# Performance work log

Hardware: AMD Instinct MI355X
Metric: run time of the kernel (lower is better)

Reference implementation:

```python
import jax, jax.numpy as jnp
import numpy as np

N = 100000
E = 3200000
IN_F = 256
OUT_F = 128
ALPHA = 0.2  # LeakyReLU negative slope


def setup_inputs() -> dict:
    key = jax.random.key(0)
    k1, k2, k3, k4, k5 = jax.random.split(key, 5)
    x = jax.random.normal(k1, (N, IN_F), dtype=jnp.float32)
    edge_row = jax.random.randint(k2, (E,), 0, N, dtype=jnp.int32)
    edge_col = jax.random.randint(k3, (E,), 0, N, dtype=jnp.int32)
    # xavier-uniform style scaling (gain 1.414)
    lim_W = 1.414 * np.sqrt(6.0 / (IN_F + OUT_F))
    W = jax.random.uniform(k4, (IN_F, OUT_F), minval=-lim_W, maxval=lim_W, dtype=jnp.float32)
    lim_a = 1.414 * np.sqrt(6.0 / (1 + 2 * OUT_F))
    a = jax.random.uniform(k5, (2 * OUT_F,), minval=-lim_a, maxval=lim_a, dtype=jnp.float32)
    return {"x": x, "edge_row": edge_row, "edge_col": edge_col, "W": W, "a": a}


def reference(x, edge_row, edge_col, W, a):
    # h = x @ W : [N, OUT_F]
    h = x @ W
    # edge score: leakyrelu([h_src || h_dst] . a) computed as two node-level dots
    a_src, a_dst = a[:OUT_F], a[OUT_F:]
    s_src = h @ a_src  # [N]
    s_dst = h @ a_dst  # [N]
    e = s_src[edge_row] + s_dst[edge_col]  # [E]
    e = jnp.where(e > 0, e, ALPHA * e)     # LeakyReLU
    # sparse softmax along dim=1 (over columns within each row -> segment by row)
    row_max = jax.ops.segment_max(e, edge_row, num_segments=N)  # [N]
    e_exp = jnp.exp(e - row_max[edge_row])
    row_sum = jax.ops.segment_sum(e_exp, edge_row, num_segments=N)  # [N]
    att = e_exp / row_sum[edge_row]  # [E]
    # sparse-dense matmul: h_prime[i] = sum_j att_ij * h[j]
    h_prime = jax.ops.segment_sum(att[:, None] * h[edge_col], edge_row, num_segments=N)
    # concat=True -> ELU
    return jax.nn.elu(h_prime)
```

## Files before the change

kernel.cpp:

```cpp
#include <hip/hip_runtime.h>
#include <hip/hip_bf16.h>
#include <math.h>

#define N_NODES 100000
#define N_EDGES 3200000
#define IN_FEAT 256
#define OUT_FEAT 128
#define ALPHA 0.2f
#define NB 782
#define NBLK 200
#define CHUNK 16000

#define SCAN_N (NB * NBLK)
#define SCAN_ELEMS 2048
#define SCAN_BLOCKS ((SCAN_N + SCAN_ELEMS - 1) / SCAN_ELEMS)
#define SCAT_IT 10

typedef __attribute__((ext_vector_type(8))) short short8;
typedef __attribute__((ext_vector_type(4))) float f32x4;

__device__ __forceinline__ ushort f2bf(float f) {
  __hip_bfloat16 h = __float2bfloat16(f);
  return __builtin_bit_cast(ushort, h);
}
__device__ __forceinline__ float bflo(uint u) { return __uint_as_float(u << 16); }
__device__ __forceinline__ float bfhi(uint u) { return __uint_as_float(u & 0xFFFF0000u); }

__global__ __launch_bounds__(256) void wt_kernel(const float* __restrict__ W,
                                                 ushort* __restrict__ Wt) {
  int id = blockIdx.x * 256 + threadIdx.x;
  int c = id >> 8;
  int k = id & 255;
  Wt[id] = f2bf(W[k * OUT_FEAT + c]);
}

#define GBM 128
#define GBK 32
#define A_LD 40
#define C_LD 136
#define HIST_BLKS NBLK

__global__ __launch_bounds__(256) void gemm_hist_kernel(const float* __restrict__ x,
                                                        const ushort* __restrict__ Wt,
                                                        const float* __restrict__ a,
                                                        const int* __restrict__ erow,
                                                        ushort* __restrict__ h16,
                                                        float* __restrict__ s_src,
                                                        float* __restrict__ s_dst,
                                                        int* __restrict__ G) {
  __shared__ union {
    struct { ushort A[GBM * A_LD]; ushort B[OUT_FEAT * A_LD]; } s;
    ushort C[GBM * C_LD];
    int hist[NB];
  } sm;
  __shared__ float sa[2 * OUT_FEAT];
  const int tid = threadIdx.x;

  if (blockIdx.x < HIST_BLKS) {
    const int b = blockIdx.x;
    for (int k = tid; k < NB; k += 256) sm.hist[k] = 0;
    __syncthreads();
    const int base = b * CHUNK;
    for (int i = base + tid; i < base + CHUNK; i += 256) atomicAdd(&sm.hist[erow[i] >> 7], 1);
    __syncthreads();
    for (int k = tid; k < NB; k += 256) G[k * NBLK + b] = sm.hist[k];
    return;
  }

  const int row0 = (blockIdx.x - HIST_BLKS) * GBM;
  const int lane = tid & 63;
  const int wave = tid >> 6;
  const int lr = lane & 15;
  const int lg = lane >> 4;

  sa[tid] = a[tid];

  f32x4 acc[2][8];
#pragma unroll
  for (int m = 0; m < 2; ++m)
#pragma unroll
    for (int n = 0; n < 8; ++n) acc[m][n] = (f32x4)(0.f);

  const int sr = tid >> 1;
  const int sh = tid & 1;
  const bool arow_ok = (row0 + sr) < N_NODES;
  const float* xg = x + (size_t)(row0 + sr) * IN_FEAT + sh * 16;
  const ushort* wg = Wt + sr * IN_FEAT + sh * 16;

  for (int ks = 0; ks < IN_FEAT / GBK; ++ks) {
    float4 f[4];
    if (arow_ok) {
#pragma unroll
      for (int i = 0; i < 4; ++i) f[i] = *(const float4*)(xg + ks * GBK + i * 4);
    } else {
#pragma unroll
      for (int i = 0; i < 4; ++i) f[i] = make_float4(0.f, 0.f, 0.f, 0.f);
    }
#pragma unroll
    for (int i = 0; i < 4; ++i) {
      uint2 p;
      p.x = (uint)f2bf(f[i].x) | ((uint)f2bf(f[i].y) << 16);
      p.y = (uint)f2bf(f[i].z) | ((uint)f2bf(f[i].w) << 16);
      *(uint2*)&sm.s.A[sr * A_LD + sh * 16 + i * 4] = p;
    }
    {
      short8 b0 = *(const short8*)(wg + ks * GBK);
      short8 b1 = *(const short8*)(wg + ks * GBK + 8);
      *(short8*)&sm.s.B[sr * A_LD + sh * 16] = b0;
      *(short8*)&sm.s.B[sr * A_LD + sh * 16 + 8] = b1;
    }
    __syncthreads();
    short8 af[2], bf[8];
#pragma unroll
    for (int m = 0; m < 2; ++m)
      af[m] = *(const short8*)&sm.s.A[(wave * 32 + m * 16 + lr) * A_LD + lg * 8];
#pragma unroll
    for (int n = 0; n < 8; ++n)
      bf[n] = *(const short8*)&sm.s.B[(n * 16 + lr) * A_LD + lg * 8];
#pragma unroll
    for (int m = 0; m < 2; ++m)
#pragma unroll
      for (int n = 0; n < 8; ++n)
        acc[m][n] = __builtin_amdgcn_mfma_f32_16x16x32_bf16(af[m], bf[n], acc[m][n], 0, 0, 0);
    __syncthreads();
  }

#pragma unroll
  for (int m = 0; m < 2; ++m)
#pragma unroll
    for (int n = 0; n < 8; ++n)
#pragma unroll
      for (int i = 0; i < 4; ++i)
        sm.C[(wave * 32 + m * 16 + lg * 4 + i) * C_LD + n * 16 + lr] = f2bf(acc[m][n][i]);
  __syncthreads();
  {
    const int row = sr;
    const bool ok = (row0 + row) < N_NODES;
    const ushort* src = &sm.C[row * C_LD + sh * 64];
    if (ok) {
      ushort* dst = h16 + (size_t)(row0 + row) * OUT_FEAT + sh * 64;
#pragma unroll
      for (int i = 0; i < 8; ++i) *(short8*)(dst + i * 8) = *(const short8*)(src + i * 8);
    }
    float ds = 0.f, dd = 0.f;
    const float* as = &sa[sh * 64];
    const float* ad = &sa[OUT_FEAT + sh * 64];
#pragma unroll
    for (int i = 0; i < 64; ++i) {
      float hv = __uint_as_float((uint)src[i] << 16);
      ds = fmaf(hv, as[i], ds);
      dd = fmaf(hv, ad[i], dd);
    }
    ds += __shfl_xor(ds, 1, 64);
    dd += __shfl_xor(dd, 1, 64);
    if (sh == 0 && ok) {
      s_src[row0 + row] = ds;
      s_dst[row0 + row] = dd;
    }
  }
}

__global__ __launch_bounds__(256) void scan1_kernel(const int* __restrict__ src,
                                                    int* __restrict__ dst,
                                                    int* __restrict__ bsum) {
  __shared__ int tsum[256];
  const int b = blockIdx.x;
  const int t = threadIdx.x;
  const int base = b * SCAN_ELEMS + t * 8;
  int v[8];
  int s = 0;
#pragma unroll
  for (int i = 0; i < 8; ++i) {
    int idx = base + i;
    v[i] = (idx < SCAN_N) ? src[idx] : 0;
    s += v[i];
  }
  tsum[t] = s;
  __syncthreads();
  for (int d = 1; d < 256; d <<= 1) {
    int u = (t >= d) ? tsum[t - d] : 0;
    __syncthreads();
    tsum[t] += u;
    __syncthreads();
  }
  int run = (t == 0) ? 0 : tsum[t - 1];
#pragma unroll
  for (int i = 0; i < 8; ++i) {
    int idx = base + i;
    if (idx < SCAN_N) dst[idx] = run;
    run += v[i];
  }
  if (t == 255) bsum[b] = tsum[255];
}

__global__ __launch_bounds__(256) void scan3_kernel(int* __restrict__ dst,
                                                    const int* __restrict__ bsum) {
  __shared__ int s[128];
  const int b = blockIdx.x;
  const int t = threadIdx.x;
  if (t < 128) s[t] = (t < SCAN_BLOCKS) ? bsum[t] : 0;
  __syncthreads();
  for (int d = 1; d < 128; d <<= 1) {
    int u = 0;
    if (t >= d && t < 128) u = s[t - d];
    __syncthreads();
    if (t < 128) s[t] += u;
    __syncthreads();
  }
  const int add = (b == 0) ? 0 : s[b - 1];
  const int base = b * SCAN_ELEMS + t * 8;
#pragma unroll
  for (int i = 0; i < 8; ++i) {
    int idx = base + i;
    if (idx < SCAN_N) dst[idx] += add;
  }
  if (b == 0 && t == 0) dst[SCAN_N] = s[SCAN_BLOCKS - 1];
}

__global__ __launch_bounds__(1024) void partition_kernel(const int* __restrict__ erow,
                                                         const int* __restrict__ ecol,
                                                         const int* __restrict__ scanG,
                                                         uint* __restrict__ packed) {
  __shared__ int cur[NB];
  const int b = blockIdx.x;
  const int t = threadIdx.x;
  for (int k = t; k < NB; k += 1024) cur[k] = scanG[k * NBLK + b];
  __syncthreads();
  const int base = b * CHUNK;
  for (int i = base + t; i < base + CHUNK; i += 1024) {
    int r = erow[i];
    int c = ecol[i];
    int pos = atomicAdd(&cur[r >> 7], 1);
    packed[pos] = ((uint)(r & 127) << 17) | (uint)c;
  }
}

__global__ __launch_bounds__(512) void bucket_scatter_kernel(const uint* __restrict__ packed,
                                                             const int* __restrict__ scanG,
                                                             int* __restrict__ offs,
                                                             int* __restrict__ scol) {
  __shared__ int cnt[128];
  __shared__ int sc[128];
  const int b = blockIdx.x;
  const int t = threadIdx.x;
  const int beg = scanG[b * NBLK];
  const int end = scanG[(b + 1) * NBLK];
  if (t < 128) cnt[t] = 0;
  __syncthreads();
  uint it[SCAT_IT];
  int nit = 0;
#pragma unroll
  for (int k = 0; k < SCAT_IT; ++k) {
    int i = beg + t + k * 512;
    if (i < end) {
      uint p = packed[i];
      it[k] = p;
      nit = k + 1;
      atomicAdd(&cnt[p >> 17], 1);
    }
  }
  __syncthreads();
  if (t < 128) sc[t] = cnt[t];
  __syncthreads();
  for (int d = 1; d < 128; d <<= 1) {
    int v = 0;
    if (t >= d && t < 128) v = sc[t - d];
    __syncthreads();
    if (t < 128) sc[t] += v;
    __syncthreads();
  }
  const int row0 = b << 7;
  if (t < 128) {
    int rstart = beg + sc[t] - cnt[t];
    if (row0 + t < N_NODES) offs[row0 + t] = rstart;
    sc[t] = rstart;
    cnt[t] = 0;
  }
  if (b == NB - 1 && t == 0) offs[N_NODES] = end;
  __syncthreads();
#pragma unroll
  for (int k = 0; k < SCAT_IT; ++k) {
    if (k < nit) {
      uint p = it[k];
      int rl = p >> 17;
      int pos = sc[rl] + atomicAdd(&cnt[rl], 1);
      scol[pos] = (int)(p & 0x1FFFFu);
    }
  }
}

__global__ __launch_bounds__(256) void attn_kernel(const ushort* __restrict__ h16,
                                                   const float* __restrict__ s_src,
                                                   const float* __restrict__ s_dst,
                                                   const int* __restrict__ offs,
                                                   const int* __restrict__ scol,
                                                   float* __restrict__ out) {
  __shared__ uint2 apair[4][128];
  const int lane = threadIdx.x & 63;
  const int w = threadIdx.x >> 6;
  const int r = blockIdx.x * 4 + w;
  const int o0 = offs[r];
  const int deg = offs[r + 1] - o0;
  const int g = lane >> 4;
  const int fo = (lane & 15) * 8;
  float* orow = out + (size_t)r * OUT_FEAT + fo;

  if (deg == 0) {
    if (g == 0) {
      *(float4*)orow = make_float4(0.f, 0.f, 0.f, 0.f);
      *(float4*)(orow + 4) = make_float4(0.f, 0.f, 0.f, 0.f);
    }
    return;
  }

  const float ssrc = s_src[r];
  const ushort* hb = h16 + fo;
  float acc[8] = {0.f, 0.f, 0.f, 0.f, 0.f, 0.f, 0.f, 0.f};

  if (deg <= 128) {
    int c0 = 0, c1 = 0;
    float p0 = -INFINITY, p1 = -INFINITY;
    if (lane < deg) {
      c0 = scol[o0 + lane];
      float e = ssrc + s_dst[c0];
      p0 = e > 0.f ? e : ALPHA * e;
    }
    if (lane + 64 < deg) {
      c1 = scol[o0 + 64 + lane];
      float e = ssrc + s_dst[c1];
      p1 = e > 0.f ? e : ALPHA * e;
    }
    float m = fmaxf(p0, p1);
#pragma unroll
    for (int off = 32; off >= 1; off >>= 1) m = fmaxf(m, __shfl_xor(m, off, 64));
    p0 = __expf(p0 - m);
    p1 = __expf(p1 - m);
    float ssum = p0 + p1;
#pragma unroll
    for (int off = 32; off >= 1; off >>= 1) ssum += __shfl_xor(ssum, off, 64);
    const float inv = 1.f / ssum;
    p0 *= inv;
    p1 *= inv;

    apair[w][lane] = make_uint2(__float_as_uint(p0), (uint)c0);
    apair[w][64 + lane] = make_uint2(__float_as_uint(p1), (uint)c1);

    const int degR = (deg + 3) & ~3;
#pragma unroll 4
    for (int j = 0; j < degR; j += 4) {
      uint2 pr = apair[w][j + g];
      float att = __uint_as_float(pr.x);
      uint4 v = *(const uint4*)(hb + (size_t)pr.y * OUT_FEAT);
      acc[0] = fmaf(att, bflo(v.x), acc[0]);
      acc[1] = fmaf(att, bfhi(v.x), acc[1]);
      acc[2] = fmaf(att, bflo(v.y), acc[2]);
      acc[3] = fmaf(att, bfhi(v.y), acc[3]);
      acc[4] = fmaf(att, bflo(v.z), acc[4]);
      acc[5] = fmaf(att, bfhi(v.z), acc[5]);
      acc[6] = fmaf(att, bflo(v.w), acc[6]);
      acc[7] = fmaf(att, bfhi(v.w), acc[7]);
    }
  } else {
    float m = -INFINITY;
    for (int j = lane; j < deg; j += 64) {
      int c = scol[o0 + j];
      float e = ssrc + s_dst[c];
      e = e > 0.f ? e : ALPHA * e;
      m = fmaxf(m, e);
    }
#pragma unroll
    for (int off = 32; off >= 1; off >>= 1) m = fmaxf(m, __shfl_xor(m, off, 64));
    float ssum = 0.f;
    for (int j = lane; j < deg; j += 64) {
      int c = scol[o0 + j];
      float e = ssrc + s_dst[c];
      e = e > 0.f ? e : ALPHA * e;
      ssum += __expf(e - m);
    }
#pragma unroll
    for (int off = 32; off >= 1; off >>= 1) ssum += __shfl_xor(ssum, off, 64);
    const float inv = 1.f / ssum;
    for (int j = 0; j < deg; j += 4) {
      int jj = j + g;
      float att = 0.f;
      int c = 0;
      if (jj < deg) {
        c = scol[o0 + jj];
        float e = ssrc + s_dst[c];
        e = e > 0.f ? e : ALPHA * e;
        att = __expf(e - m) * inv;
      }
      uint4 v = *(const uint4*)(hb + (size_t)c * OUT_FEAT);
      acc[0] = fmaf(att, bflo(v.x), acc[0]);
      acc[1] = fmaf(att, bfhi(v.x), acc[1]);
      acc[2] = fmaf(att, bflo(v.y), acc[2]);
      acc[3] = fmaf(att, bfhi(v.y), acc[3]);
      acc[4] = fmaf(att, bflo(v.z), acc[4]);
      acc[5] = fmaf(att, bfhi(v.z), acc[5]);
      acc[6] = fmaf(att, bflo(v.w), acc[6]);
      acc[7] = fmaf(att, bfhi(v.w), acc[7]);
    }
  }

#pragma unroll
  for (int k = 0; k < 8; ++k) {
    acc[k] += __shfl_xor(acc[k], 16, 64);
    acc[k] += __shfl_xor(acc[k], 32, 64);
  }
  if (g == 0) {
#pragma unroll
    for (int k = 0; k < 8; ++k) acc[k] = acc[k] > 0.f ? acc[k] : expm1f(acc[k]);
    *(float4*)orow = make_float4(acc[0], acc[1], acc[2], acc[3]);
    *(float4*)(orow + 4) = make_float4(acc[4], acc[5], acc[6], acc[7]);
  }
}

extern "C" void kernel_launch(void* const* d_in, const int* in_sizes, int n_in,
                              void* d_out, int out_size, void* d_ws, size_t ws_size,
                              hipStream_t stream) {
  const float* x = (const float*)d_in[0];
  const int* erow = (const int*)d_in[1];
  const int* ecol = (const int*)d_in[2];
  const float* W = (const float*)d_in[3];
  const float* a = (const float*)d_in[4];
  float* out = (float*)d_out;

  char* ws = (char*)d_ws;
  size_t off = 0;
  auto alloc = [&](size_t bytes) {
    void* p = ws + off;
    off = (off + bytes + 255) & ~(size_t)255;
    return p;
  };
  const int M_PAD = 782 * GBM;
  ushort* h16 = (ushort*)alloc((size_t)M_PAD * OUT_FEAT * sizeof(ushort));
  ushort* Wt = (ushort*)alloc((size_t)IN_FEAT * OUT_FEAT * sizeof(ushort));
  float* s_src = (float*)alloc((size_t)N_NODES * sizeof(float));
  float* s_dst = (float*)alloc((size_t)N_NODES * sizeof(float));
  int* offs = (int*)alloc((size_t)(N_NODES + 1) * sizeof(int));
  int* G = (int*)alloc((size_t)SCAN_N * sizeof(int));
  int* scanG = (int*)alloc((size_t)(SCAN_N + 1) * sizeof(int));
  int* bsum = (int*)alloc((size_t)SCAN_BLOCKS * sizeof(int));
  uint* packed = (uint*)alloc((size_t)N_EDGES * sizeof(uint));
  int* scol = (int*)alloc((size_t)N_EDGES * sizeof(int));

  wt_kernel<<<(IN_FEAT * OUT_FEAT) / 256, 256, 0, stream>>>(W, Wt);
  gemm_hist_kernel<<<HIST_BLKS + 782, 256, 0, stream>>>(x, Wt, a, erow, h16, s_src, s_dst, G);
  scan1_kernel<<<SCAN_BLOCKS, 256, 0, stream>>>(G, scanG, bsum);
  scan3_kernel<<<SCAN_BLOCKS, 256, 0, stream>>>(scanG, bsum);
  partition_kernel<<<NBLK, 1024, 0, stream>>>(erow, ecol, scanG, packed);
  bucket_scatter_kernel<<<NB, 512, 0, stream>>>(packed, scanG, offs, scol);
  attn_kernel<<<N_NODES / 4, 256, 0, stream>>>(h16, s_src, s_dst, offs, scol, out);
}
```

Measured before the change: 214.4 us.

## Keep full W tile in LDS, load x fragments directly to registers

Result: slower. 274.8 us (+28.2%).

```diff
diff --git a/kernel.cpp b/kernel.cpp
--- a/kernel.cpp
+++ b/kernel.cpp
@@ -26,6 +26,15 @@
 __device__ __forceinline__ float bflo(uint u) { return __uint_as_float(u << 16); }
 __device__ __forceinline__ float bfhi(uint u) { return __uint_as_float(u & 0xFFFF0000u); }
 
+__device__ __forceinline__ short8 pack_bf8(float4 a, float4 b) {
+  union { short8 s; uint u[4]; } r;
+  r.u[0] = (uint)f2bf(a.x) | ((uint)f2bf(a.y) << 16);
+  r.u[1] = (uint)f2bf(a.z) | ((uint)f2bf(a.w) << 16);
+  r.u[2] = (uint)f2bf(b.x) | ((uint)f2bf(b.y) << 16);
+  r.u[3] = (uint)f2bf(b.z) | ((uint)f2bf(b.w) << 16);
+  return r.s;
+}
+
 __global__ __launch_bounds__(256) void wt_kernel(const float* __restrict__ W,
                                                  ushort* __restrict__ Wt) {
   int id = blockIdx.x * 256 + threadIdx.x;
@@ -36,7 +45,7 @@
 
 #define GBM 128
 #define GBK 32
-#define A_LD 40
+#define B_LD 264
 #define C_LD 136
 #define HIST_BLKS NBLK
 
@@ -49,7 +58,7 @@
                                                         float* __restrict__ s_dst,
                                                         int* __restrict__ G) {
   __shared__ union {
-    struct { ushort A[GBM * A_LD]; ushort B[OUT_FEAT * A_LD]; } s;
+    ushort B[OUT_FEAT * B_LD];
     ushort C[GBM * C_LD];
     int hist[NB];
   } sm;
@@ -75,56 +84,47 @@
 
   sa[tid] = a[tid];
 
+  for (int i = tid; i < (OUT_FEAT * IN_FEAT) / 8; i += 256) {
+    int col = i >> 5;
+    int kc = (i & 31) << 3;
+    *(short8*)&sm.B[col * B_LD + kc] = *(const short8*)(Wt + col * IN_FEAT + kc);
+  }
+  __syncthreads();
+
   f32x4 acc[2][8];
 #pragma unroll
   for (int m = 0; m < 2; ++m)
 #pragma unroll
     for (int n = 0; n < 8; ++n) acc[m][n] = (f32x4)(0.f);
 
-  const int sr = tid >> 1;
-  const int sh = tid & 1;
-  const bool arow_ok = (row0 + sr) < N_NODES;
-  const float* xg = x + (size_t)(row0 + sr) * IN_FEAT + sh * 16;
-  const ushort* wg = Wt + sr * IN_FEAT + sh * 16;
-
+  const int arow0 = row0 + wave * 32 + lr;
+  const int arow1 = arow0 + 16;
+  const float* xg0 = x + (size_t)arow0 * IN_FEAT + lg * 8;
+  const float* xg1 = x + (size_t)arow1 * IN_FEAT + lg * 8;
+  const bool ok0 = arow0 < N_NODES;
+  const bool ok1 = arow1 < N_NODES;
+  const float4 z4 = make_float4(0.f, 0.f, 0.f, 0.f);
+
+#pragma unroll
   for (int ks = 0; ks < IN_FEAT / GBK; ++ks) {
-    float4 f[4];
-    if (arow_ok) {
-#pragma unroll
-      for (int i = 0; i < 4; ++i) f[i] = *(const float4*)(xg + ks * GBK + i * 4);
-    } else {
-#pragma unroll
-      for (int i = 0; i < 4; ++i) f[i] = make_float4(0.f, 0.f, 0.f, 0.f);
-    }
-#pragma unroll
-    for (int i = 0; i < 4; ++i) {
-      uint2 p;
-      p.x = (uint)f2bf(f[i].x) | ((uint)f2bf(f[i].y) << 16);
-      p.y = (uint)f2bf(f[i].z) | ((uint)f2bf(f[i].w) << 16);
-      *(uint2*)&sm.s.A[sr * A_LD + sh * 16 + i * 4] = p;
-    }
-    {
-      short8 b0 = *(const short8*)(wg + ks * GBK);
-      short8 b1 = *(const short8*)(wg + ks * GBK + 8);
-      *(short8*)&sm.s.B[sr * A_LD + sh * 16] = b0;
-      *(short8*)&sm.s.B[sr * A_LD + sh * 16 + 8] = b1;
-    }
-    __syncthreads();
-    short8 af[2], bf[8];
-#pragma unroll
-    for (int m = 0; m < 2; ++m)
-      af[m] = *(const short8*)&sm.s.A[(wave * 32 + m * 16 + lr) * A_LD + lg * 8];
+    float4 a0 = ok0 ? *(const float4*)(xg0 + ks * GBK) : z4;
+    float4 a1 = ok0 ? *(const float4*)(xg0 + ks * GBK + 4) : z4;
+    float4 b0 = ok1 ? *(const float4*)(xg1 + ks * GBK) : z4;
+    float4 b1 = ok1 ? *(const float4*)(xg1 + ks * GBK + 4) : z4;
+    short8 af0 = pack_bf8(a0, a1);
+    short8 af1 = pack_bf8(b0, b1);
+    short8 bf[8];
 #pragma unroll
     for (int n = 0; n < 8; ++n)
-      bf[n] = *(const short8*)&sm.s.B[(n * 16 + lr) * A_LD + lg * 8];
-#pragma unroll
-    for (int m = 0; m < 2; ++m)
-#pragma unroll
-      for (int n = 0; n < 8; ++n)
-        acc[m][n] = __builtin_amdgcn_mfma_f32_16x16x32_bf16(af[m], bf[n], acc[m][n], 0, 0, 0);
-    __syncthreads();
-  }
-
+      bf[n] = *(const short8*)&sm.B[(n * 16 + lr) * B_LD + ks * GBK + lg * 8];
+#pragma unroll
+    for (int n = 0; n < 8; ++n) {
+      acc[0][n] = __builtin_amdgcn_mfma_f32_16x16x32_bf16(af0, bf[n], acc[0][n], 0, 0, 0);
+      acc[1][n] = __builtin_amdgcn_mfma_f32_16x16x32_bf16(af1, bf[n], acc[1][n], 0, 0, 0);
+    }
+  }
+
+  __syncthreads();
 #pragma unroll
   for (int m = 0; m < 2; ++m)
 #pragma unroll
@@ -134,7 +134,8 @@
         sm.C[(wave * 32 + m * 16 + lg * 4 + i) * C_LD + n * 16 + lr] = f2bf(acc[m][n][i]);
   __syncthreads();
   {
-    const int row = sr;
+    const int row = tid >> 1;
+    const int sh = tid & 1;
     const bool ok = (row0 + row) < N_NODES;
     const ushort* src = &sm.C[row * C_LD + sh * 64];
     if (ok) {
@@ -227,11 +228,16 @@
   for (int k = t; k < NB; k += 1024) cur[k] = scanG[k * NBLK + b];
   __syncthreads();
   const int base = b * CHUNK;
-  for (int i = base + t; i < base + CHUNK; i += 1024) {
-    int r = erow[i];
-    int c = ecol[i];
-    int pos = atomicAdd(&cur[r >> 7], 1);
-    packed[pos] = ((uint)(r & 127) << 17) | (uint)c;
+  for (int i = base + t * 4; i < base + CHUNK; i += 4096) {
+    int4 r4 = *(const int4*)(erow + i);
+    int4 c4 = *(const int4*)(ecol + i);
+#pragma unroll
+    for (int k = 0; k < 4; ++k) {
+      int r = (&r4.x)[k];
+      int c = (&c4.x)[k];
+      int pos = atomicAdd(&cur[r >> 7], 1);
+      packed[pos] = ((uint)(r & 127) << 17) | (uint)c;
+    }
   }
 }
 
```
